# Kernel tuning notes

Measured on AMD Instinct MI355X. Metric: run time of the kernel, lower is better.

## Reference

```python
import jax, jax.numpy as jnp
import numpy as np

RES = 32  # voxel grid resolution per axis (cfg.MODEL.NEURAL_POINTS.VOXEL_RES)


def upsample_ac(x, s):
    """Bilinear upsample with align_corners=True. x: [B,C,h,w] -> [B,C,h*s,w*s]."""
    if s == 1:
        return x
    B, C, h, w = x.shape
    H, W = h * s, w * s
    ys = jnp.arange(H, dtype=x.dtype) * ((h - 1) / (H - 1))
    xs = jnp.arange(W, dtype=x.dtype) * ((w - 1) / (W - 1))
    y0 = jnp.floor(ys).astype(jnp.int32)
    x0 = jnp.floor(xs).astype(jnp.int32)
    y1 = jnp.minimum(y0 + 1, h - 1)
    x1 = jnp.minimum(x0 + 1, w - 1)
    wy = (ys - y0.astype(x.dtype))[:, None]  # [H,1]
    wx = (xs - x0.astype(x.dtype))[None, :]  # [1,W]
    top = x[:, :, y0, :]
    bot = x[:, :, y1, :]
    a = top[..., x0]; b = top[..., x1]; c = bot[..., x0]; d = bot[..., x1]
    return (a * (1 - wx) + b * wx) * (1 - wy) + (c * (1 - wx) + d * wx) * wy


def vox_closest(pos):
    """construct_vox_points_closest: per occupied voxel, index of point closest to
    the voxel's point centroid. pos: [N,3] -> [RES^3] int32 indices."""
    N = pos.shape[0]
    Vn = RES ** 3
    mn = pos.min(0)
    mx = pos.max(0)
    vsz = (mx - mn) / RES  # obtain_voxel_size_based_grid_res
    coord = jnp.clip(jnp.floor((pos - mn) / vsz).astype(jnp.int32), 0, RES - 1)
    vid = (coord[:, 0] * RES + coord[:, 1]) * RES + coord[:, 2]  # [N]
    cnt = jax.ops.segment_sum(jnp.ones((N,), pos.dtype), vid, Vn)
    cen = jax.ops.segment_sum(pos, vid, Vn) / jnp.maximum(cnt, 1.0)[:, None]
    d = jnp.sum((pos - cen[vid]) ** 2, axis=-1)  # [N] dist^2 to own-voxel centroid
    dmin = jax.ops.segment_min(d, vid, Vn)
    cand = jnp.where(d <= dmin[vid], jnp.arange(N, dtype=jnp.int32), N)
    midx = jax.ops.segment_min(cand, vid, Vn)
    return jnp.where(midx >= N, 0, midx)  # guard (rare) empty voxels


def reference(rgb, f1, f2, f3, points_pos, points_dir, W1, b1, W2, b2, points_mask):
    V, _, H, W = rgb.shape
    N = V * H * W
    C = 59
    # valid_index = where(points_mask == 1) (mask is all ones -> identity gather)
    valid = jnp.nonzero(points_mask[0] == 1, size=N, fill_value=0)[0]
    pos = points_pos[0, valid]          # [N,3]
    pdir = points_dir[0, valid]         # [N,3]
    # project_point_feats: upsample each pyramid level to full res, concat channels
    ups = [upsample_ac(rgb, 1), upsample_ac(f1, 2), upsample_ac(f2, 4), upsample_ac(f3, 8)]
    pif = jnp.concatenate(ups, axis=1)                       # [V,59,H,W]
    pif = jnp.transpose(pif, (0, 2, 3, 1)).reshape(N, C)     # [N,59]
    color = jax.lax.stop_gradient(jnp.transpose(rgb, (0, 2, 3, 1)).reshape(N, 3))
    pif = pif[valid]
    color = color[valid]
    emb = jnp.concatenate([pif, pdir], axis=-1)              # [N,62]
    midx = vox_closest(pos)                                  # [32768]
    sel_emb = emb[midx]
    sel_pos = pos[midx]
    sel_color = color[midx]
    sel_dir = pdir[midx]
    # point_mlp (premlp_init): 62 -> 256 -> 256
    h = jax.nn.relu(sel_emb @ W1 + b1)
    points_embedding = h @ W2 + b2
    return points_embedding, sel_pos, sel_color, sel_dir


def setup_inputs() -> dict:
    key = jax.random.key(0)
    ks = jax.random.split(key, 10)
    V, H, W = 8, 240, 320
    N = V * H * W
    return {
        "rgb": jax.random.uniform(ks[0], (V, 3, H, W), jnp.float32),
        "f1": jax.random.normal(ks[1], (V, 8, H // 2, W // 2), jnp.float32),
        "f2": jax.random.normal(ks[2], (V, 16, H // 4, W // 4), jnp.float32),
        "f3": jax.random.normal(ks[3], (V, 32, H // 8, W // 8), jnp.float32),
        "points_pos": jax.random.uniform(ks[4], (1, N, 3), jnp.float32),
        "points_dir": jax.random.normal(ks[5], (1, N, 3), jnp.float32),
        "W1": jax.random.normal(ks[6], (62, 256), jnp.float32) * 0.05,
        "b1": jnp.zeros((256,), jnp.float32),
        "W2": jax.random.normal(ks[7], (256, 256), jnp.float32) * 0.05,
        "b2": jnp.zeros((256,), jnp.float32),
        "points_mask": jnp.ones((1, N), jnp.int32),
    }
```

## Files before the change

kernel.cpp:

```cpp
#include <hip/hip_runtime.h>
#include <hip/hip_bf16.h>
#include <limits.h>
#include <stddef.h>

#define NPTS   614400
#define RESV   32
#define NVOX   (RESV*RESV*RESV)
#define IMG_H  240
#define IMG_W  320
#define IMG_HW (IMG_H*IMG_W)
#define INF    __builtin_inff()
#define CAP    48
#define SPILLCAP 4096

typedef __attribute__((ext_vector_type(8))) short short8;
typedef __attribute__((ext_vector_type(4))) short s16x4;
typedef __attribute__((ext_vector_type(4))) float f32x4;

__device__ __forceinline__ float fadd_(float a, float b){
#pragma clang fp contract(off)
  return a + b;
}
__device__ __forceinline__ float fsub_(float a, float b){
#pragma clang fp contract(off)
  return a - b;
}
__device__ __forceinline__ float fmul_(float a, float b){
#pragma clang fp contract(off)
  return a * b;
}
__device__ __forceinline__ float fdiv_(float a, float b){
#pragma clang fp contract(off)
  return a / b;
}

__device__ __forceinline__ short f2bf(float x){
  __hip_bfloat16 h = __float2bfloat16(x);
  return *reinterpret_cast<short*>(&h);
}

__device__ __forceinline__ void atomicMinF(float* addr, float v){
  if (v >= 0.f) atomicMin((int*)addr, __float_as_int(v));
  else          atomicMax((unsigned int*)addr, __float_as_uint(v));
}
__device__ __forceinline__ void atomicMaxF(float* addr, float v){
  if (v >= 0.f) atomicMax((int*)addr, __float_as_int(v));
  else          atomicMin((unsigned int*)addr, __float_as_uint(v));
}

__device__ __forceinline__ int voxid3(float x, float y, float z,
                                      const unsigned* __restrict__ mnmx){
  float p[3] = {x, y, z};
  int v = 0;
  #pragma unroll
  for (int c = 0; c < 3; c++){
    float mn  = __uint_as_float(mnmx[c]);
    float mx  = __uint_as_float(mnmx[3+c]);
    float vsz = fdiv_(fsub_(mx, mn), 32.0f);
    float t   = fdiv_(fsub_(p[c], mn), vsz);
    int cc = (int)floorf(t);
    cc = min(max(cc, 0), RESV-1);
    v = v*RESV + cc;
  }
  return v;
}

__global__ void k_init0(unsigned* __restrict__ mnmx){
  int i = threadIdx.x;
  if (i < 3){
    mnmx[i]   = 0x7f800000u;
    mnmx[3+i] = 0xff800000u;
  }
  if (i == 3) mnmx[6] = 0u;
}

__global__ void k_prep(int* __restrict__ cnt, unsigned* __restrict__ mnmx,
                       const float* __restrict__ W1, const float* __restrict__ W2,
                       short* __restrict__ W1t, short* __restrict__ W2t,
                       const float* __restrict__ pos){
  int gid = blockIdx.x*blockDim.x + threadIdx.x;
  if (gid < NVOX) cnt[gid] = 0;
  if (gid < 256*64){
    int n = gid >> 6, k = gid & 63;
    W1t[gid] = (k < 62) ? f2bf(W1[k*256 + n]) : (short)0;
  } else if (gid < 256*64 + 256*256){
    int j = gid - 256*64;
    int n = j >> 8, k = j & 255;
    W2t[j] = f2bf(W2[k*256 + n]);
  }

  const f32x4* p4 = (const f32x4*)pos;
  float mn[3] = {  INF,  INF,  INF };
  float mx[3] = { -INF, -INF, -INF };
  int stride = gridDim.x*blockDim.x;
  for (int t = gid; t < NPTS/4; t += stride){
    f32x4 a = p4[3*t+0], b = p4[3*t+1], c = p4[3*t+2];
    mn[0] = fminf(mn[0], fminf(fminf(a.x, a.w), fminf(b.z, c.y)));
    mx[0] = fmaxf(mx[0], fmaxf(fmaxf(a.x, a.w), fmaxf(b.z, c.y)));
    mn[1] = fminf(mn[1], fminf(fminf(a.y, b.x), fminf(b.w, c.z)));
    mx[1] = fmaxf(mx[1], fmaxf(fmaxf(a.y, b.x), fmaxf(b.w, c.z)));
    mn[2] = fminf(mn[2], fminf(fminf(a.z, b.y), fminf(c.x, c.w)));
    mx[2] = fmaxf(mx[2], fmaxf(fmaxf(a.z, b.y), fmaxf(c.x, c.w)));
  }
  #pragma unroll
  for (int off = 32; off >= 1; off >>= 1){
    #pragma unroll
    for (int c = 0; c < 3; c++){
      mn[c] = fminf(mn[c], __shfl_down(mn[c], off, 64));
      mx[c] = fmaxf(mx[c], __shfl_down(mx[c], off, 64));
    }
  }
  __shared__ float smn[4][3], smx[4][3];
  int lane = threadIdx.x & 63, w = threadIdx.x >> 6;
  if (lane == 0){
    #pragma unroll
    for (int c = 0; c < 3; c++){ smn[w][c] = mn[c]; smx[w][c] = mx[c]; }
  }
  __syncthreads();
  if (threadIdx.x < 3){
    int c = threadIdx.x;
    float a = fminf(fminf(smn[0][c], smn[1][c]), fminf(smn[2][c], smn[3][c]));
    float b = fmaxf(fmaxf(smx[0][c], smx[1][c]), fmaxf(smx[2][c], smx[3][c]));
    atomicMinF((float*)&mnmx[c],   a);
    atomicMaxF((float*)&mnmx[3+c], b);
  }
}

__global__ void k_scatter(const float* __restrict__ pos, const unsigned* __restrict__ mnmx,
                          int* __restrict__ cnt, f32x4* __restrict__ slots,
                          int* __restrict__ spill_v, f32x4* __restrict__ spill_pay){
  int t = blockIdx.x*blockDim.x + threadIdx.x;
  const f32x4* p4 = (const f32x4*)pos;
  f32x4 a = p4[3*t+0], b = p4[3*t+1], c = p4[3*t+2];
  float X[4] = {a.x, a.w, b.z, c.y};
  float Y[4] = {a.y, b.x, b.w, c.z};
  float Z[4] = {a.z, b.y, c.x, c.w};
  #pragma unroll
  for (int j = 0; j < 4; j++){
    int i = 4*t + j;
    int v = voxid3(X[j], Y[j], Z[j], mnmx);
    int p = atomicAdd(&cnt[v], 1);
    f32x4 s; s.x = X[j]; s.y = Y[j]; s.z = Z[j]; s.w = __int_as_float(i);
    if (p < CAP){
      slots[(size_t)v*CAP + p] = s;
    } else {
      int sp = atomicAdd((int*)&mnmx[6], 1);
      if (sp < SPILLCAP){ spill_v[sp] = v; spill_pay[sp] = s; }
    }
  }
}

__launch_bounds__(256)
__global__ void k_voxfull(const int* __restrict__ cnt, const f32x4* __restrict__ slots,
                          const int* __restrict__ spill_v, const f32x4* __restrict__ spill_pay,
                          const unsigned* __restrict__ mnmx,
                          const float* __restrict__ pos,
                          const float* __restrict__ pdir, const float* __restrict__ rgb,
                          const float* __restrict__ f1, const float* __restrict__ f2,
                          const float* __restrict__ f3,
                          float* __restrict__ selpos, float* __restrict__ selcol,
                          float* __restrict__ seldir, short* __restrict__ emb){
  int lane = threadIdx.x & 63;
  int v = blockIdx.x*4 + (threadIdx.x >> 6);
  int n = cnt[v];
  int m = 0;

  if (n > CAP){
    if (lane == 0){
      int sc = min((int)mnmx[6], SPILLCAP);
      float sx = 0.f, sy = 0.f, sz = 0.f; int last = -1;
      for (int i = 0; i < n; i++){
        int best = INT_MAX; float bx = 0.f, by = 0.f, bz = 0.f;
        for (int j = 0; j < CAP; j++){
          f32x4 s = slots[(size_t)v*CAP + j]; int id = __float_as_int(s.w);
          if (id > last && id < best){ best = id; bx = s.x; by = s.y; bz = s.z; }
        }
        for (int j = 0; j < sc; j++){
          if (spill_v[j] == v){
            f32x4 s = spill_pay[j]; int id = __float_as_int(s.w);
            if (id > last && id < best){ best = id; bx = s.x; by = s.y; bz = s.z; }
          }
        }
        sx = fadd_(sx, bx); sy = fadd_(sy, by); sz = fadd_(sz, bz);
        last = best;
      }
      float cf = (float)n;
      float cx = fdiv_(sx, cf), cy = fdiv_(sy, cf), cz = fdiv_(sz, cf);
      float dmin = INF; int mm = 0;
      for (int j = 0; j < CAP + sc; j++){
        f32x4 s; int ok = 1;
        if (j < CAP) s = slots[(size_t)v*CAP + j];
        else { ok = (spill_v[j-CAP] == v); s = spill_pay[j-CAP]; }
        if (!ok) continue;
        int id = __float_as_int(s.w);
        float dx = fsub_(s.x, cx), dy = fsub_(s.y, cy), dz = fsub_(s.z, cz);
        float d  = fadd_(fadd_(fmul_(dx,dx), fmul_(dy,dy)), fmul_(dz,dz));
        if (d < dmin || (d == dmin && id < mm)){ dmin = d; mm = id; }
      }
      m = mm;
    }
    m = __shfl(m, 0, 64);
  } else {
    f32x4 s;
    int key = INT_MAX;
    if (lane < n){ s = slots[(size_t)v*CAP + lane]; key = __float_as_int(s.w); }
    int src = lane;
    #pragma unroll
    for (int k = 2; k <= 64; k <<= 1){
      #pragma unroll
      for (int j = k >> 1; j >= 1; j >>= 1){
        int ok = __shfl_xor(key, j, 64);
        int os = __shfl_xor(src, j, 64);
        bool up    = ((lane & k) == 0);
        bool lower = ((lane & j) == 0);
        bool sw = (lower == up) ? (ok < key) : (ok > key);
        if (sw){ key = ok; src = os; }
      }
    }
    float px = __shfl(s.x, src, 64);
    float py = __shfl(s.y, src, 64);
    float pz = __shfl(s.z, src, 64);

    float sx = 0.f, sy = 0.f, sz = 0.f;
    for (int i = 0; i < n; i++){
      sx = fadd_(sx, __shfl(px, i, 64));
      sy = fadd_(sy, __shfl(py, i, 64));
      sz = fadd_(sz, __shfl(pz, i, 64));
    }
    float cf = fmaxf((float)n, 1.0f);
    float cx = fdiv_(sx, cf), cy = fdiv_(sy, cf), cz = fdiv_(sz, cf);

    float bd = INF; int bi = 0;
    if (lane < n){
      float dx = fsub_(px, cx), dy = fsub_(py, cy), dz = fsub_(pz, cz);
      bd = fadd_(fadd_(fmul_(dx,dx), fmul_(dy,dy)), fmul_(dz,dz));
      bi = key;
    }
    #pragma unroll
    for (int off = 32; off >= 1; off >>= 1){
      float od = __shfl_xor(bd, off, 64);
      int   oi = __shfl_xor(bi, off, 64);
      if (od < bd || (od == bd && oi < bi)){ bd = od; bi = oi; }
    }
    m = bi;
  }

  int img = m / IMG_HW;
  int rem = m - img*IMG_HW;
  int y = rem / IMG_W;
  int x = rem - y*IMG_W;
  int ch = lane;
  float val;
  if (ch < 3){
    val = rgb[((img*3 + ch)*IMG_H + y)*IMG_W + x];
    selcol[3*v+ch] = val;
    selpos[3*v+ch] = pos[3*m+ch];
  } else if (ch < 59){
    int lvl = (ch >= 27) ? 2 : ((ch >= 11) ? 1 : 0);
    const float* f = (lvl == 0) ? f1 : ((lvl == 1) ? f2 : f3);
    int c   = ch - ((lvl == 0) ? 3 : ((lvl == 1) ? 11 : 27));
    int C   = 8 << lvl;
    int h   = 120 >> lvl, w = 160 >> lvl;
    float ry = (lvl == 0) ? (119.0f/239.0f) : ((lvl == 1) ? (59.0f/239.0f) : (29.0f/239.0f));
    float rx = (lvl == 0) ? (159.0f/319.0f) : ((lvl == 1) ? (79.0f/319.0f) : (39.0f/319.0f));
    float ys = (float)y * ry;
    float xs = (float)x * rx;
    int y0 = (int)floorf(ys);
    int x0 = (int)floorf(xs);
    int y1 = min(y0+1, h-1);
    int x1 = min(x0+1, w-1);
    float wy = ys - (float)y0;
    float wx = xs - (float)x0;
    const float* plane = f + ((size_t)img*C + c)*(size_t)(h*w);
    float aa = plane[y0*w + x0];
    float bb = plane[y0*w + x1];
    float cc = plane[y1*w + x0];
    float dd = plane[y1*w + x1];
    val = (aa*(1.f-wx) + bb*wx)*(1.f-wy) + (cc*(1.f-wx) + dd*wx)*wy;
  } else if (ch < 62){
    val = pdir[3*m + (ch-59)];
    seldir[3*v+(ch-59)] = val;
  } else {
    val = 0.f;
  }
  emb[(size_t)v*64 + ch] = f2bf(val);
}

#define MLP_BLOCKS 512
#define MLP_TILES  (NVOX/16/MLP_BLOCKS)
__launch_bounds__(256, 2)
__global__ void k_mlp(const short* __restrict__ emb, const short* __restrict__ W1t,
                      const float* __restrict__ b1f, const short* __restrict__ W2t,
                      const float* __restrict__ b2f, float* __restrict__ out){
  __shared__ short Hs[16][264];
  int t    = threadIdx.x;
  int lane = t & 63;
  int wv   = t >> 6;
  int m    = lane & 15;
  int q    = lane >> 4;

  short8 w1f[4][2], w2f[4][8];
  float  b1r[4][4], b2r[4];
  #pragma unroll
  for (int nt = 0; nt < 4; nt++){
    int n = wv*64 + nt*16 + m;
    #pragma unroll
    for (int kq = 0; kq < 2; kq++)
      w1f[nt][kq] = *(const short8*)&W1t[(size_t)n*64 + kq*32 + q*8];
    #pragma unroll
    for (int kq = 0; kq < 8; kq++)
      w2f[nt][kq] = *(const short8*)&W2t[(size_t)n*256 + kq*32 + q*8];
    #pragma unroll
    for (int i = 0; i < 4; i++)
      b1r[nt][i] = b1f[wv*64 + nt*16 + q*4 + i];
    b2r[nt] = b2f[n];
  }

  for (int tt = 0; tt < MLP_TILES; tt++){
    int row0 = (blockIdx.x*MLP_TILES + tt)*16;

    short8 ef0 = *(const short8*)&emb[(size_t)(row0 + m)*64 + q*8];
    short8 ef1 = *(const short8*)&emb[(size_t)(row0 + m)*64 + 32 + q*8];

    #pragma unroll
    for (int nt = 0; nt < 4; nt++){
      f32x4 c = {0.f, 0.f, 0.f, 0.f};
      c = __builtin_amdgcn_mfma_f32_16x16x32_bf16(w1f[nt][0], ef0, c, 0, 0, 0);
      c = __builtin_amdgcn_mfma_f32_16x16x32_bf16(w1f[nt][1], ef1, c, 0, 0, 0);
      s16x4 hv;
      #pragma unroll
      for (int i = 0; i < 4; i++)
        hv[i] = f2bf(fmaxf(c[i] + b1r[nt][i], 0.f));
      *(s16x4*)&Hs[m][wv*64 + nt*16 + q*4] = hv;
    }
    __syncthreads();

    f32x4 acc[4] = {{0,0,0,0},{0,0,0,0},{0,0,0,0},{0,0,0,0}};
    #pragma unroll
    for (int kq = 0; kq < 8; kq++){
      short8 af = *(const short8*)&Hs[m][kq*32 + q*8];
      #pragma unroll
      for (int nt = 0; nt < 4; nt++)
        acc[nt] = __builtin_amdgcn_mfma_f32_16x16x32_bf16(af, w2f[nt][kq], acc[nt], 0, 0, 0);
    }
    __syncthreads();

    #pragma unroll
    for (int nt = 0; nt < 4; nt++){
      int n = wv*64 + nt*16 + m;
      #pragma unroll
      for (int i = 0; i < 4; i++)
        out[(size_t)(row0 + q*4 + i)*256 + n] = acc[nt][i] + b2r[nt];
    }
  }
}

extern "C" void kernel_launch(void* const* d_in, const int* in_sizes, int n_in,
                              void* d_out, int out_size, void* d_ws, size_t ws_size,
                              hipStream_t stream){
  const float* rgb  = (const float*)d_in[0];
  const float* f1   = (const float*)d_in[1];
  const float* f2   = (const float*)d_in[2];
  const float* f3   = (const float*)d_in[3];
  const float* pos  = (const float*)d_in[4];
  const float* pdir = (const float*)d_in[5];
  const float* W1   = (const float*)d_in[6];
  const float* b1   = (const float*)d_in[7];
  const float* W2   = (const float*)d_in[8];
  const float* b2   = (const float*)d_in[9];

  float* out      = (float*)d_out;
  float* out_emb  = out;
  float* out_pos  = out + (size_t)NVOX*256;
  float* out_col  = out_pos + (size_t)NVOX*3;
  float* out_dir  = out_col + (size_t)NVOX*3;

  char* w = (char*)d_ws;
  unsigned* mnmx  = (unsigned*)w;  w += 64;
  int*   cnt      = (int*)w;       w += (size_t)NVOX*4;
  short* W1t      = (short*)w;     w += (size_t)256*64*2;
  short* W2t      = (short*)w;     w += (size_t)256*256*2;
  short* emb      = (short*)w;     w += (size_t)NVOX*64*2;
  int*   spill_v  = (int*)w;       w += (size_t)SPILLCAP*4 + 48;
  f32x4* spill_p  = (f32x4*)w;     w += (size_t)SPILLCAP*16;
  f32x4* slots    = (f32x4*)w;     w += (size_t)NVOX*CAP*16;

  k_init0   <<<1,       64, 0, stream>>>(mnmx);
  k_prep    <<<512,    256, 0, stream>>>(cnt, mnmx, W1, W2, W1t, W2t, pos);
  k_scatter <<<NPTS/1024, 256, 0, stream>>>(pos, mnmx, cnt, slots, spill_v, spill_p);
  k_voxfull <<<NVOX/4, 256, 0, stream>>>(cnt, slots, spill_v, spill_p, mnmx,
                                         pos, pdir, rgb, f1, f2, f3,
                                         out_pos, out_col, out_dir, emb);
  k_mlp     <<<MLP_BLOCKS, 256, 0, stream>>>(emb, W1t, b1, W2t, b2, out_emb);
}
```

Before: 212.6 us.

## Store point indices in voxel slots and reduce min/max via per-block partials

```diff
diff --git a/kernel.cpp b/kernel.cpp
--- a/kernel.cpp
+++ b/kernel.cpp
@@ -10,12 +10,13 @@
 #define IMG_W  320
 #define IMG_HW (IMG_H*IMG_W)
 #define INF    __builtin_inff()
-#define CAP    48
+#define CAP    64
 #define SPILLCAP 4096
 
 typedef __attribute__((ext_vector_type(8))) short short8;
 typedef __attribute__((ext_vector_type(4))) short s16x4;
 typedef __attribute__((ext_vector_type(4))) float f32x4;
+typedef float f32x4u __attribute__((ext_vector_type(4), aligned(4)));
 
 __device__ __forceinline__ float fadd_(float a, float b){
 #pragma clang fp contract(off)
@@ -39,47 +40,14 @@
   return *reinterpret_cast<short*>(&h);
 }
 
-__device__ __forceinline__ void atomicMinF(float* addr, float v){
-  if (v >= 0.f) atomicMin((int*)addr, __float_as_int(v));
-  else          atomicMax((unsigned int*)addr, __float_as_uint(v));
-}
-__device__ __forceinline__ void atomicMaxF(float* addr, float v){
-  if (v >= 0.f) atomicMax((int*)addr, __float_as_int(v));
-  else          atomicMin((unsigned int*)addr, __float_as_uint(v));
-}
-
-__device__ __forceinline__ int voxid3(float x, float y, float z,
-                                      const unsigned* __restrict__ mnmx){
-  float p[3] = {x, y, z};
-  int v = 0;
-  #pragma unroll
-  for (int c = 0; c < 3; c++){
-    float mn  = __uint_as_float(mnmx[c]);
-    float mx  = __uint_as_float(mnmx[3+c]);
-    float vsz = fdiv_(fsub_(mx, mn), 32.0f);
-    float t   = fdiv_(fsub_(p[c], mn), vsz);
-    int cc = (int)floorf(t);
-    cc = min(max(cc, 0), RESV-1);
-    v = v*RESV + cc;
-  }
-  return v;
-}
-
-__global__ void k_init0(unsigned* __restrict__ mnmx){
-  int i = threadIdx.x;
-  if (i < 3){
-    mnmx[i]   = 0x7f800000u;
-    mnmx[3+i] = 0xff800000u;
-  }
-  if (i == 3) mnmx[6] = 0u;
-}
-
-__global__ void k_prep(int* __restrict__ cnt, unsigned* __restrict__ mnmx,
+__global__ void k_prep(int* __restrict__ cnt, int* __restrict__ spillcnt,
                        const float* __restrict__ W1, const float* __restrict__ W2,
                        short* __restrict__ W1t, short* __restrict__ W2t,
-                       const float* __restrict__ pos){
+                       const float* __restrict__ pos,
+                       f32x4* __restrict__ pmin, f32x4* __restrict__ pmax){
   int gid = blockIdx.x*blockDim.x + threadIdx.x;
   if (gid < NVOX) cnt[gid] = 0;
+  if (gid == 0) *spillcnt = 0;
   if (gid < 256*64){
     int n = gid >> 6, k = gid & 63;
     W1t[gid] = (k < 62) ? f2bf(W1[k*256 + n]) : (short)0;
@@ -117,18 +85,59 @@
     for (int c = 0; c < 3; c++){ smn[w][c] = mn[c]; smx[w][c] = mx[c]; }
   }
   __syncthreads();
-  if (threadIdx.x < 3){
-    int c = threadIdx.x;
-    float a = fminf(fminf(smn[0][c], smn[1][c]), fminf(smn[2][c], smn[3][c]));
-    float b = fmaxf(fmaxf(smx[0][c], smx[1][c]), fmaxf(smx[2][c], smx[3][c]));
-    atomicMinF((float*)&mnmx[c],   a);
-    atomicMaxF((float*)&mnmx[3+c], b);
-  }
-}
-
-__global__ void k_scatter(const float* __restrict__ pos, const unsigned* __restrict__ mnmx,
-                          int* __restrict__ cnt, f32x4* __restrict__ slots,
-                          int* __restrict__ spill_v, f32x4* __restrict__ spill_pay){
+  if (threadIdx.x == 0){
+    f32x4 a, b;
+    a.x = fminf(fminf(smn[0][0], smn[1][0]), fminf(smn[2][0], smn[3][0]));
+    a.y = fminf(fminf(smn[0][1], smn[1][1]), fminf(smn[2][1], smn[3][1]));
+    a.z = fminf(fminf(smn[0][2], smn[1][2]), fminf(smn[2][2], smn[3][2]));
+    a.w = 0.f;
+    b.x = fmaxf(fmaxf(smx[0][0], smx[1][0]), fmaxf(smx[2][0], smx[3][0]));
+    b.y = fmaxf(fmaxf(smx[0][1], smx[1][1]), fmaxf(smx[2][1], smx[3][1]));
+    b.z = fmaxf(fmaxf(smx[0][2], smx[1][2]), fmaxf(smx[2][2], smx[3][2]));
+    b.w = 0.f;
+    pmin[blockIdx.x] = a;
+    pmax[blockIdx.x] = b;
+  }
+}
+
+__device__ __forceinline__ void reduce_minmax(const f32x4* __restrict__ pmin,
+                                              const f32x4* __restrict__ pmax,
+                                              float mn[3], float vsz[3]){
+  int t = threadIdx.x;
+  f32x4 a = pmin[t], b = pmin[t+256];
+  f32x4 c = pmax[t], d = pmax[t+256];
+  float lmn[3] = { fminf(a.x,b.x), fminf(a.y,b.y), fminf(a.z,b.z) };
+  float lmx[3] = { fmaxf(c.x,d.x), fmaxf(c.y,d.y), fmaxf(c.z,d.z) };
+  #pragma unroll
+  for (int off = 32; off >= 1; off >>= 1){
+    #pragma unroll
+    for (int k = 0; k < 3; k++){
+      lmn[k] = fminf(lmn[k], __shfl_xor(lmn[k], off, 64));
+      lmx[k] = fmaxf(lmx[k], __shfl_xor(lmx[k], off, 64));
+    }
+  }
+  __shared__ float smn[4][3], smx[4][3];
+  int lane = t & 63, w = t >> 6;
+  if (lane == 0){
+    #pragma unroll
+    for (int k = 0; k < 3; k++){ smn[w][k] = lmn[k]; smx[w][k] = lmx[k]; }
+  }
+  __syncthreads();
+  #pragma unroll
+  for (int k = 0; k < 3; k++){
+    mn[k] = fminf(fminf(smn[0][k], smn[1][k]), fminf(smn[2][k], smn[3][k]));
+    float mx = fmaxf(fmaxf(smx[0][k], smx[1][k]), fmaxf(smx[2][k], smx[3][k]));
+    vsz[k] = fdiv_(fsub_(mx, mn[k]), 32.0f);
+  }
+}
+
+__global__ void k_scatter(const float* __restrict__ pos,
+                          const f32x4* __restrict__ pmin, const f32x4* __restrict__ pmax,
+                          int* __restrict__ cnt, int* __restrict__ slots,
+                          int* __restrict__ spillcnt, int2* __restrict__ spill){
+  float mn[3], vsz[3];
+  reduce_minmax(pmin, pmax, mn, vsz);
+
   int t = blockIdx.x*blockDim.x + threadIdx.x;
   const f32x4* p4 = (const f32x4*)pos;
   f32x4 a = p4[3*t+0], b = p4[3*t+1], c = p4[3*t+2];
@@ -138,22 +147,28 @@
   #pragma unroll
   for (int j = 0; j < 4; j++){
     int i = 4*t + j;
-    int v = voxid3(X[j], Y[j], Z[j], mnmx);
+    float P[3] = {X[j], Y[j], Z[j]};
+    int v = 0;
+    #pragma unroll
+    for (int k = 0; k < 3; k++){
+      float tt = fdiv_(fsub_(P[k], mn[k]), vsz[k]);
+      int cc = (int)floorf(tt);
+      cc = min(max(cc, 0), RESV-1);
+      v = v*RESV + cc;
+    }
     int p = atomicAdd(&cnt[v], 1);
-    f32x4 s; s.x = X[j]; s.y = Y[j]; s.z = Z[j]; s.w = __int_as_float(i);
     if (p < CAP){
-      slots[(size_t)v*CAP + p] = s;
+      slots[v*CAP + p] = i;
     } else {
-      int sp = atomicAdd((int*)&mnmx[6], 1);
-      if (sp < SPILLCAP){ spill_v[sp] = v; spill_pay[sp] = s; }
+      int sp = atomicAdd(spillcnt, 1);
+      if (sp < SPILLCAP){ int2 e; e.x = v; e.y = i; spill[sp] = e; }
     }
   }
 }
 
 __launch_bounds__(256)
-__global__ void k_voxfull(const int* __restrict__ cnt, const f32x4* __restrict__ slots,
-                          const int* __restrict__ spill_v, const f32x4* __restrict__ spill_pay,
-                          const unsigned* __restrict__ mnmx,
+__global__ void k_voxfull(const int* __restrict__ cnt, const int* __restrict__ slots,
+                          const int* __restrict__ spillcnt, const int2* __restrict__ spill,
                           const float* __restrict__ pos,
                           const float* __restrict__ pdir, const float* __restrict__ rgb,
                           const float* __restrict__ f1, const float* __restrict__ f2,
@@ -164,36 +179,39 @@
   int v = blockIdx.x*4 + (threadIdx.x >> 6);
   int n = cnt[v];
   int m = 0;
+  unsigned long long ball = 0;
+  float px = 0.f, py = 0.f, pz = 0.f;
 
   if (n > CAP){
     if (lane == 0){
-      int sc = min((int)mnmx[6], SPILLCAP);
+      int sc = min(*spillcnt, SPILLCAP);
       float sx = 0.f, sy = 0.f, sz = 0.f; int last = -1;
       for (int i = 0; i < n; i++){
-        int best = INT_MAX; float bx = 0.f, by = 0.f, bz = 0.f;
+        int best = INT_MAX;
         for (int j = 0; j < CAP; j++){
-          f32x4 s = slots[(size_t)v*CAP + j]; int id = __float_as_int(s.w);
-          if (id > last && id < best){ best = id; bx = s.x; by = s.y; bz = s.z; }
+          int id = slots[v*CAP + j];
+          if (id > last && id < best) best = id;
         }
         for (int j = 0; j < sc; j++){
-          if (spill_v[j] == v){
-            f32x4 s = spill_pay[j]; int id = __float_as_int(s.w);
-            if (id > last && id < best){ best = id; bx = s.x; by = s.y; bz = s.z; }
-          }
+          int2 e = spill[j];
+          if (e.x == v && e.y > last && e.y < best) best = e.y;
         }
-        sx = fadd_(sx, bx); sy = fadd_(sy, by); sz = fadd_(sz, bz);
+        sx = fadd_(sx, pos[3*best+0]);
+        sy = fadd_(sy, pos[3*best+1]);
+        sz = fadd_(sz, pos[3*best+2]);
         last = best;
       }
       float cf = (float)n;
       float cx = fdiv_(sx, cf), cy = fdiv_(sy, cf), cz = fdiv_(sz, cf);
       float dmin = INF; int mm = 0;
       for (int j = 0; j < CAP + sc; j++){
-        f32x4 s; int ok = 1;
-        if (j < CAP) s = slots[(size_t)v*CAP + j];
-        else { ok = (spill_v[j-CAP] == v); s = spill_pay[j-CAP]; }
+        int id; int ok = 1;
+        if (j < CAP) id = slots[v*CAP + j];
+        else { int2 e = spill[j-CAP]; ok = (e.x == v); id = e.y; }
         if (!ok) continue;
-        int id = __float_as_int(s.w);
-        float dx = fsub_(s.x, cx), dy = fsub_(s.y, cy), dz = fsub_(s.z, cz);
+        float dx = fsub_(pos[3*id+0], cx);
+        float dy = fsub_(pos[3*id+1], cy);
+        float dz = fsub_(pos[3*id+2], cz);
         float d  = fadd_(fadd_(fmul_(dx,dx), fmul_(dy,dy)), fmul_(dz,dz));
         if (d < dmin || (d == dmin && id < mm)){ dmin = d; mm = id; }
       }
@@ -201,9 +219,17 @@
     }
     m = __shfl(m, 0, 64);
   } else {
-    f32x4 s;
     int key = INT_MAX;
-    if (lane < n){ s = slots[(size_t)v*CAP + lane]; key = __float_as_int(s.w); }
+    float gx = 0.f, gy = 0.f, gz = 0.f;
+    if (lane < n){
+      key = slots[v*CAP + lane];
+      if (key < NPTS-1){
+        f32x4u q = *(const f32x4u*)&pos[3*key];
+        gx = q.x; gy = q.y; gz = q.z;
+      } else {
+        gx = pos[3*key+0]; gy = pos[3*key+1]; gz = pos[3*key+2];
+      }
+    }
     int src = lane;
     #pragma unroll
     for (int k = 2; k <= 64; k <<= 1){
@@ -217,9 +243,9 @@
         if (sw){ key = ok; src = os; }
       }
     }
-    float px = __shfl(s.x, src, 64);
-    float py = __shfl(s.y, src, 64);
-    float pz = __shfl(s.z, src, 64);
+    px = __shfl(gx, src, 64);
+    py = __shfl(gy, src, 64);
+    pz = __shfl(gz, src, 64);
 
     float sx = 0.f, sy = 0.f, sz = 0.f;
     for (int i = 0; i < n; i++){
@@ -243,6 +269,15 @@
       if (od < bd || (od == bd && oi < bi)){ bd = od; bi = oi; }
     }
     m = bi;
+    ball = __ballot(lane < n && key == m);
+  }
+
+  float wx_ = 0.f, wy_ = 0.f, wz_ = 0.f;
+  if (ball){
+    int wl = (int)(__ffsll((long long)ball) - 1);
+    wx_ = __shfl(px, wl, 64);
+    wy_ = __shfl(py, wl, 64);
+    wz_ = __shfl(pz, wl, 64);
   }
 
   int img = m / IMG_HW;
@@ -254,7 +289,8 @@
   if (ch < 3){
     val = rgb[((img*3 + ch)*IMG_H + y)*IMG_W + x];
     selcol[3*v+ch] = val;
-    selpos[3*v+ch] = pos[3*m+ch];
+    float sp = ball ? ((ch == 0) ? wx_ : (ch == 1) ? wy_ : wz_) : pos[3*m+ch];
+    selpos[3*v+ch] = sp;
   } else if (ch < 59){
     int lvl = (ch >= 27) ? 2 : ((ch >= 11) ? 1 : 0);
     const float* f = (lvl == 0) ? f1 : ((lvl == 1) ? f2 : f3);
@@ -376,19 +412,19 @@
   float* out_dir  = out_col + (size_t)NVOX*3;
 
   char* w = (char*)d_ws;
-  unsigned* mnmx  = (unsigned*)w;  w += 64;
+  int*   spillcnt = (int*)w;       w += 64;
+  f32x4* pmin     = (f32x4*)w;     w += (size_t)512*16;
+  f32x4* pmax     = (f32x4*)w;     w += (size_t)512*16;
   int*   cnt      = (int*)w;       w += (size_t)NVOX*4;
   short* W1t      = (short*)w;     w += (size_t)256*64*2;
   short* W2t      = (short*)w;     w += (size_t)256*256*2;
   short* emb      = (short*)w;     w += (size_t)NVOX*64*2;
-  int*   spill_v  = (int*)w;       w += (size_t)SPILLCAP*4 + 48;
-  f32x4* spill_p  = (f32x4*)w;     w += (size_t)SPILLCAP*16;
-  f32x4* slots    = (f32x4*)w;     w += (size_t)NVOX*CAP*16;
-
-  k_init0   <<<1,       64, 0, stream>>>(mnmx);
-  k_prep    <<<512,    256, 0, stream>>>(cnt, mnmx, W1, W2, W1t, W2t, pos);
-  k_scatter <<<NPTS/1024, 256, 0, stream>>>(pos, mnmx, cnt, slots, spill_v, spill_p);
-  k_voxfull <<<NVOX/4, 256, 0, stream>>>(cnt, slots, spill_v, spill_p, mnmx,
+  int2*  spill    = (int2*)w;      w += (size_t)SPILLCAP*8;
+  int*   slots    = (int*)w;       w += (size_t)NVOX*CAP*4;
+
+  k_prep    <<<512,    256, 0, stream>>>(cnt, spillcnt, W1, W2, W1t, W2t, pos, pmin, pmax);
+  k_scatter <<<NPTS/1024, 256, 0, stream>>>(pos, pmin, pmax, cnt, slots, spillcnt, spill);
+  k_voxfull <<<NVOX/4, 256, 0, stream>>>(cnt, slots, spillcnt, spill,
                                          pos, pdir, rgb, f1, f2, f3,
                                          out_pos, out_col, out_dir, emb);
   k_mlp     <<<MLP_BLOCKS, 256, 0, stream>>>(emb, W1t, b1, W2t, b2, out_emb);
```

New measurement: 198.2 us. 1.07x faster.
